# Performance work log

Measured on AMD Instinct MI355X. Metric: run time of the kernel, lower is better.

## Reference

```python
import jax, jax.numpy as jnp
import numpy as np

B, N, HID = 2, 2048, 1024
NH = 16
HD = HID // NH

def setup_inputs() -> dict:
    key = jax.random.key(0)
    ks = jax.random.split(key, 5)
    s = 0.02
    return {
        "hidden_states": jax.random.normal(ks[0], (B, N, HID), jnp.float32),
        "attention_mask": jnp.zeros((B, 1, 1, N), jnp.float32),
        "Wq": jax.random.normal(ks[1], (HID, HID), jnp.float32) * s,
        "bq": jnp.zeros((HID,), jnp.float32),
        "Wk": jax.random.normal(ks[2], (HID, HID), jnp.float32) * s,
        "bk": jnp.zeros((HID,), jnp.float32),
        "Wv": jax.random.normal(ks[3], (HID, HID), jnp.float32) * s,
        "bv": jnp.zeros((HID,), jnp.float32),
    }

def reference(hidden_states, attention_mask, Wq, bq, Wk, bk, Wv, bv):
    b, n, _ = hidden_states.shape
    def split_heads(t):  # [b,n,hid] -> [b,h,n,d]
        return t.reshape(b, n, NH, HD).transpose(0, 2, 1, 3)
    q = split_heads(hidden_states @ Wq.T + bq)
    k = split_heads(hidden_states @ Wk.T + bk)
    v = split_heads(hidden_states @ Wv.T + bv)
    scores = jnp.einsum('bhnd,bhmd->bhnm', q, k) / jnp.sqrt(jnp.float32(HD)).astype(q.dtype)
    scores = scores + attention_mask
    scores = jnp.maximum(scores, jnp.finfo(scores.dtype).min)
    probs = jax.nn.softmax(scores, axis=-1)
    out = jnp.einsum('bhnm,bhmd->bhnd', probs, v)
    return out.transpose(0, 2, 1, 3).reshape(b, n, NH * HD)
```

## Files before the change

### kernel.cpp

```cpp
#include <hip/hip_runtime.h>

typedef unsigned short u16;
typedef unsigned int   u32;
typedef __attribute__((ext_vector_type(8))) short bf16x8;
typedef __attribute__((ext_vector_type(4))) float f32x4;
typedef __attribute__((ext_vector_type(2))) unsigned int u32x2;

__device__ __forceinline__ float bf2f(u16 u) { return __uint_as_float(((u32)u) << 16); }
__device__ __forceinline__ u16 f2bf(float f) {
    return (u16)((__float_as_uint(f) + 0x8000u) >> 16);
}
__device__ __forceinline__ u32 cvt_pk_bf16(float lo, float hi) {
    u32 r;
    asm("v_cvt_pk_bf16_f32 %0, %1, %2" : "=v"(r) : "v"(lo), "v"(hi));
    return r;
}
__device__ __forceinline__ void gload16(const void* g, void* l) {
    __builtin_amdgcn_global_load_lds((const __attribute__((address_space(1))) void*)g,
                                     (__attribute__((address_space(3))) void*)l, 16, 0, 0);
}
#define VMCNT(n) asm volatile("s_waitcnt vmcnt(" #n ")" ::: "memory")

struct us4 { u16 x, y, z, w; };
__global__ void cvt_all(const float* __restrict__ hs, const float* __restrict__ wq,
                        const float* __restrict__ wk, const float* __restrict__ wv,
                        u16* __restrict__ dst)
{
    int i = blockIdx.x * blockDim.x + threadIdx.x;
    const int stride = gridDim.x * blockDim.x;
    us4* d4 = (us4*)dst;
    for (; i < 1835008; i += stride) {
        const float4* s4;
        int j = i;
        if (j < 1048576)      { s4 = (const float4*)hs; }
        else if (j < 1310720) { s4 = (const float4*)wq; j -= 1048576; }
        else if (j < 1572864) { s4 = (const float4*)wk; j -= 1310720; }
        else                  { s4 = (const float4*)wv; j -= 1572864; }
        float4 v = s4[j];
        us4 o;
        o.x = f2bf(v.x); o.y = f2bf(v.y); o.z = f2bf(v.z); o.w = f2bf(v.w);
        d4[i] = o;
    }
}

__global__ __launch_bounds__(256) void qkv_gemm(
    const u16* __restrict__ hs,
    const u16* __restrict__ Wq, const u16* __restrict__ Wk, const u16* __restrict__ Wv,
    const float* __restrict__ bq, const float* __restrict__ bk, const float* __restrict__ bv,
    u16* __restrict__ oq, u16* __restrict__ ok, u16* __restrict__ ovt)
{
    __shared__ u16 smem[32768];
    u16* sA0 = smem;
    u16* sB0 = smem + 8192;
    u16* sA1 = smem + 16384;
    u16* sB1 = smem + 24576;

    const int tid  = threadIdx.x;
    const int lane = tid & 63;
    const int w    = tid >> 6;
    const int c15  = lane & 15;
    const int q4   = lane >> 4;
    const int mat  = blockIdx.x >> 3;
    const int cb   = blockIdx.x & 7;
    const int rb   = blockIdx.y;
    const int wr   = w >> 1, wc = w & 1;

    const u16*   W    = (mat == 0) ? Wq : (mat == 1 ? Wk : Wv);
    const float* bias = (mat == 0) ? bq : (mat == 1 ? bk : bv);

    f32x4 acc[4][4] = {};

    const int rs = tid >> 3;
    const int cs = ((tid & 7) ^ (rs & 7)) * 8;
    const u16* gA = hs + (rb * 128) * 1024;
    const u16* gB = W + (cb * 128) * 1024;

    auto stageQ = [&](u16* dA, u16* dB, int kb) {
#pragma unroll
        for (int p = 0; p < 4; ++p)
            gload16(gA + (rs + 32 * p) * 1024 + kb + cs, dA + p * 2048 + w * 512);
#pragma unroll
        for (int p = 0; p < 4; ++p)
            gload16(gB + (rs + 32 * p) * 1024 + kb + cs, dB + p * 2048 + w * 512);
    };

    auto computeQ = [&](const u16* sA, const u16* sB) {
        __builtin_amdgcn_s_setprio(1);
#pragma unroll
        for (int kk = 0; kk < 2; ++kk) {
            const int cpos = ((kk * 4 + q4) ^ (c15 & 7)) * 8;
            bf16x8 af[4], bf[4];
#pragma unroll
            for (int mt = 0; mt < 4; ++mt)
                af[mt] = *(const bf16x8*)(sA + (wr * 64 + mt * 16 + c15) * 64 + cpos);
#pragma unroll
            for (int nt = 0; nt < 4; ++nt)
                bf[nt] = *(const bf16x8*)(sB + (wc * 64 + nt * 16 + c15) * 64 + cpos);
#pragma unroll
            for (int mt = 0; mt < 4; ++mt)
#pragma unroll
                for (int nt = 0; nt < 4; ++nt)
                    acc[mt][nt] = __builtin_amdgcn_mfma_f32_16x16x32_bf16(
                        af[mt], bf[nt], acc[mt][nt], 0, 0, 0);
        }
        __builtin_amdgcn_s_setprio(0);
    };

    stageQ(sA0, sB0, 0);
    stageQ(sA1, sB1, 64);

#pragma unroll 1
    for (int T = 0; T < 14; T += 2) {
        VMCNT(8);
        __builtin_amdgcn_s_barrier();
        __builtin_amdgcn_sched_barrier(0);
        computeQ(sA0, sB0);
        __builtin_amdgcn_s_barrier();
        __builtin_amdgcn_sched_barrier(0);
        stageQ(sA0, sB0, (T + 2) * 64);

        VMCNT(8);
        __builtin_amdgcn_s_barrier();
        __builtin_amdgcn_sched_barrier(0);
        computeQ(sA1, sB1);
        __builtin_amdgcn_s_barrier();
        __builtin_amdgcn_sched_barrier(0);
        stageQ(sA1, sB1, (T + 3) * 64);
    }
    VMCNT(8);
    __builtin_amdgcn_s_barrier();
    __builtin_amdgcn_sched_barrier(0);
    computeQ(sA0, sB0);
    VMCNT(0);
    __builtin_amdgcn_s_barrier();
    __builtin_amdgcn_sched_barrier(0);
    computeQ(sA1, sB1);

    __syncthreads();
    const int h = cb * 2 + wc;
    float bvv[4];
#pragma unroll
    for (int nt = 0; nt < 4; ++nt)
        bvv[nt] = bias[cb * 128 + wc * 64 + nt * 16 + c15];

    u16* sc = smem + w * 4608;
    if (mat != 2) {
        u16* dst = (mat == 0) ? oq : ok;
#pragma unroll
        for (int mt = 0; mt < 4; ++mt)
#pragma unroll
            for (int nt = 0; nt < 4; ++nt)
#pragma unroll
                for (int rr = 0; rr < 4; ++rr)
                    sc[(mt * 16 + q4 * 4 + rr) * 72 + nt * 16 + c15] =
                        f2bf(acc[mt][nt][rr] + bvv[nt]);
#pragma unroll
        for (int p = 0; p < 8; ++p) {
            const int s = p * 64 + lane;
            const int rl = s >> 3, oct = (s & 7) * 8;
            bf16x8 vv = *(const bf16x8*)(sc + rl * 72 + oct);
            const int n = rb * 128 + wr * 64 + rl;
            const int bb = n >> 11, nn = n & 2047;
            *(bf16x8*)(dst + (((bb * 16 + h) * 2048) + nn) * 64 + oct) = vv;
        }
    } else {
#pragma unroll
        for (int mt = 0; mt < 4; ++mt)
#pragma unroll
            for (int nt = 0; nt < 4; ++nt)
#pragma unroll
                for (int rr = 0; rr < 4; ++rr)
                    sc[(nt * 16 + c15) * 72 + mt * 16 + q4 * 4 + rr] =
                        f2bf(acc[mt][nt][rr] + bvv[nt]);
#pragma unroll
        for (int p = 0; p < 8; ++p) {
            const int s = p * 64 + lane;
            const int dr = s >> 3, noct = (s & 7) * 8;
            bf16x8 vv = *(const bf16x8*)(sc + dr * 72 + noct);
            const int n0 = rb * 128 + wr * 64 + noct;
            const int bb = n0 >> 11, nn = n0 & 2047;
            *(bf16x8*)(ovt + ((bb * 16 + h) * 64 + dr) * 2048 + nn) = vv;
        }
    }
}

__global__ __launch_bounds__(256, 2) void attn(
    const u16* __restrict__ qm, const u16* __restrict__ km, const u16* __restrict__ vtm,
    const float* __restrict__ mask, float* __restrict__ out)
{
    __shared__ u16 sK0[8192];
    __shared__ u16 sV0[8192];
    __shared__ u16 sK1[8192];
    __shared__ u16 sV1[8192];

    const int tid = threadIdx.x, lane = tid & 63, w = tid >> 6;
    const int c15 = lane & 15, q4 = lane >> 4;
    const int bh = blockIdx.x;
    const int qt = blockIdx.y;
    const int b = bh >> 4;

    bf16x8 qf[2][2];
    const u16* qbase = qm + (bh * 2048 + qt * 128 + w * 32) * 64;
#pragma unroll
    for (int rt = 0; rt < 2; ++rt)
#pragma unroll
        for (int kt = 0; kt < 2; ++kt)
            qf[rt][kt] = *(const bf16x8*)(qbase + (rt * 16 + c15) * 64 + kt * 32 + q4 * 8);

    float l_acc[2] = {0.f, 0.f};
    f32x4 accO[2][4] = {};

    const u16* kbase  = km  + bh * 2048 * 64;
    const u16* vtbase = vtm + bh * 64 * 2048;

    const int rK   = tid >> 3;
    const int colK = ((tid & 7) ^ (rK & 7)) * 8;
    const int prK  = (rK & 3) | ((rK & 0x0C) << 1) | ((rK & 0x10) >> 2);
    const int rV   = tid >> 4;
    const int colV = ((tid & 15) ^ (rV & 7)) * 8;
    const int ldsW = w * 512;

    const float* mbase = mask + b * 2048 + 8 * q4;

    auto stage = [&](u16* dK, u16* dV, int TT) {
        const u16* kg = kbase + TT * 128 * 64;
        const u16* vg = vtbase + TT * 128;
#pragma unroll
        for (int p = 0; p < 4; ++p)
            gload16(kg + (prK + 32 * p) * 64 + colK, dK + p * 2048 + ldsW);
#pragma unroll
        for (int p = 0; p < 4; ++p)
            gload16(vg + (rV + 16 * p) * 2048 + colV, dV + p * 2048 + ldsW);
    };

    auto compute64 = [&](const u16* sKh, const u16* sVb, int pcBase, int kb) {
        float mkv[4][4];
#pragma unroll
        for (int t = 0; t < 4; ++t) {
            float4 m4 = *(const float4*)(mbase + kb + 32 * (t >> 1) + 4 * (t & 1));
            mkv[t][0] = m4.x * 1.4426950408889634f;
            mkv[t][1] = m4.y * 1.4426950408889634f;
            mkv[t][2] = m4.z * 1.4426950408889634f;
            mkv[t][3] = m4.w * 1.4426950408889634f;
        }

        f32x4 accST[4][2] = {};
        __builtin_amdgcn_s_setprio(1);
#pragma unroll
        for (int kt = 0; kt < 2; ++kt) {
            bf16x8 kf[4];
#pragma unroll
            for (int t = 0; t < 4; ++t) {
                const int cpos = (kt * 4 + q4) ^ (c15 & 7);
                kf[t] = *(const bf16x8*)(sKh + (t * 16 + c15) * 64 + cpos * 8);
            }
#pragma unroll
            for (int t = 0; t < 4; ++t)
#pragma unroll
                for (int rt = 0; rt < 2; ++rt)
                    accST[t][rt] = __builtin_amdgcn_mfma_f32_16x16x32_bf16(
                        kf[t], qf[rt][kt], accST[t][rt], 0, 0, 0);
        }
        __builtin_amdgcn_s_setprio(0);

        u32 pu[4][2][2];
#pragma unroll
        for (int t = 0; t < 4; ++t)
#pragma unroll
            for (int rt = 0; rt < 2; ++rt) {
                float p[4];
#pragma unroll
                for (int rr = 0; rr < 4; ++rr) {
                    p[rr] = __builtin_amdgcn_exp2f(
                        fmaf(accST[t][rt][rr], 0.18033688011112042f, mkv[t][rr]));
                    l_acc[rt] += p[rr];
                }
                pu[t][rt][0] = cvt_pk_bf16(p[0], p[1]);
                pu[t][rt][1] = cvt_pk_bf16(p[2], p[3]);
            }

        __builtin_amdgcn_s_setprio(1);
#pragma unroll
        for (int g = 0; g < 2; ++g) {
            bf16x8 vB[4];
#pragma unroll
            for (int nt = 0; nt < 4; ++nt) {
                const int d = nt * 16 + c15;
                const int pc = pcBase + ((4 * g + q4) ^ (d & 7));
                vB[nt] = *(const bf16x8*)(sVb + d * 128 + pc * 8);
            }
#pragma unroll
            for (int rt = 0; rt < 2; ++rt) {
                union { bf16x8 v; u32 u[4]; } ta;
                ta.u[0] = pu[2 * g][rt][0];
                ta.u[1] = pu[2 * g][rt][1];
                ta.u[2] = pu[2 * g + 1][rt][0];
                ta.u[3] = pu[2 * g + 1][rt][1];
#pragma unroll
                for (int nt = 0; nt < 4; ++nt)
                    accO[rt][nt] = __builtin_amdgcn_mfma_f32_16x16x32_bf16(
                        ta.v, vB[nt], accO[rt][nt], 0, 0, 0);
            }
        }
        __builtin_amdgcn_s_setprio(0);
    };

    stage(sK0, sV0, 0);
    stage(sK1, sV1, 1);

#pragma unroll 1
    for (int T = 0; T < 14; T += 2) {
        VMCNT(8);
        __builtin_amdgcn_s_barrier();
        __builtin_amdgcn_sched_barrier(0);
        compute64(sK0, sV0, 0, T * 128);
        compute64(sK0 + 64 * 64, sV0, 8, T * 128 + 64);
        __builtin_amdgcn_s_barrier();
        __builtin_amdgcn_sched_barrier(0);
        stage(sK0, sV0, T + 2);

        VMCNT(8);
        __builtin_amdgcn_s_barrier();
        __builtin_amdgcn_sched_barrier(0);
        compute64(sK1, sV1, 0, (T + 1) * 128);
        compute64(sK1 + 64 * 64, sV1, 8, (T + 1) * 128 + 64);
        __builtin_amdgcn_s_barrier();
        __builtin_amdgcn_sched_barrier(0);
        stage(sK1, sV1, T + 3);
    }
    VMCNT(8);
    __builtin_amdgcn_s_barrier();
    __builtin_amdgcn_sched_barrier(0);
    compute64(sK0, sV0, 0, 14 * 128);
    compute64(sK0 + 64 * 64, sV0, 8, 14 * 128 + 64);
    VMCNT(0);
    __builtin_amdgcn_s_barrier();
    __builtin_amdgcn_sched_barrier(0);
    compute64(sK1, sV1, 0, 15 * 128);
    compute64(sK1 + 64 * 64, sV1, 8, 15 * 128 + 64);

#pragma unroll
    for (int rt = 0; rt < 2; ++rt) {
        l_acc[rt] += __shfl_xor(l_acc[rt], 16);
        l_acc[rt] += __shfl_xor(l_acc[rt], 32);
    }

    const int h = bh & 15;
#pragma unroll
    for (int rt = 0; rt < 2; ++rt) {
        float inv[4];
#pragma unroll
        for (int rr = 0; rr < 4; ++rr)
            inv[rr] = 1.0f / __shfl(l_acc[rt], q4 * 4 + rr);
#pragma unroll
        for (int nt = 0; nt < 4; ++nt)
#pragma unroll
            for (int rr = 0; rr < 4; ++rr) {
                const int qrow = qt * 128 + w * 32 + rt * 16 + q4 * 4 + rr;
                const int d = nt * 16 + c15;
                out[(b * 2048 + qrow) * 1024 + h * 64 + d] = accO[rt][nt][rr] * inv[rr];
            }
    }
}

extern "C" void kernel_launch(void* const* d_in, const int* in_sizes, int n_in,
                              void* d_out, int out_size, void* d_ws, size_t ws_size,
                              hipStream_t stream)
{
    const float* hs   = (const float*)d_in[0];
    const float* mask = (const float*)d_in[1];
    const float* Wq   = (const float*)d_in[2];
    const float* bq   = (const float*)d_in[3];
    const float* Wk   = (const float*)d_in[4];
    const float* bk   = (const float*)d_in[5];
    const float* Wv   = (const float*)d_in[6];
    const float* bv   = (const float*)d_in[7];

    u16* ws   = (u16*)d_ws;
    u16* qw   = ws;
    u16* kw   = ws + 4194304;
    u16* vtw  = ws + 8388608;
    u16* hsb  = ws + 12582912;
    u16* wqb  = ws + 16777216;
    u16* wkb  = ws + 17825792;
    u16* wvb  = ws + 18874368;

    cvt_all<<<1024, 256, 0, stream>>>(hs, Wq, Wk, Wv, hsb);

    qkv_gemm<<<dim3(24, 32), 256, 0, stream>>>(hsb, wqb, wkb, wvb, bq, bk, bv, qw, kw, vtw);
    attn<<<dim3(32, 16), 256, 0, stream>>>(qw, kw, vtw, mask, (float*)d_out);
}
```

Baseline: 162.3 us.

## Shrink attention blocks to 128 threads with 64-query, 64-key tiles

The attention kernel now uses two waves per block covering 64 query rows instead of four waves covering 128. The launch grid doubles to 1024 blocks. K/V tiles shrink to 64 keys per stage, which halves LDS per block and doubles the number of pipeline iterations. The aim is more blocks in flight and better CU occupancy and load balance. In exchange, each block runs twice as many barriers and staging rounds, and K/V get reloaded from global/L2 twice as often in total. The exp sum is also reassociated into a pairwise add.

```diff
diff --git a/kernel.cpp b/kernel.cpp
--- a/kernel.cpp
+++ b/kernel.cpp
@@ -4,7 +4,6 @@
 typedef unsigned int   u32;
 typedef __attribute__((ext_vector_type(8))) short bf16x8;
 typedef __attribute__((ext_vector_type(4))) float f32x4;
-typedef __attribute__((ext_vector_type(2))) unsigned int u32x2;
 
 __device__ __forceinline__ float bf2f(u16 u) { return __uint_as_float(((u32)u) << 16); }
 __device__ __forceinline__ u16 f2bf(float f) {
@@ -184,14 +183,14 @@
     }
 }
 
-__global__ __launch_bounds__(256, 2) void attn(
+__global__ __launch_bounds__(128, 2) void attn(
     const u16* __restrict__ qm, const u16* __restrict__ km, const u16* __restrict__ vtm,
     const float* __restrict__ mask, float* __restrict__ out)
 {
-    __shared__ u16 sK0[8192];
-    __shared__ u16 sV0[8192];
-    __shared__ u16 sK1[8192];
-    __shared__ u16 sV1[8192];
+    __shared__ u16 sK0[4096];
+    __shared__ u16 sV0[4096];
+    __shared__ u16 sK1[4096];
+    __shared__ u16 sV1[4096];
 
     const int tid = threadIdx.x, lane = tid & 63, w = tid >> 6;
     const int c15 = lane & 15, q4 = lane >> 4;
@@ -200,7 +199,7 @@
     const int b = bh >> 4;
 
     bf16x8 qf[2][2];
-    const u16* qbase = qm + (bh * 2048 + qt * 128 + w * 32) * 64;
+    const u16* qbase = qm + (bh * 2048 + qt * 64 + w * 32) * 64;
 #pragma unroll
     for (int rt = 0; rt < 2; ++rt)
 #pragma unroll
@@ -213,27 +212,31 @@
     const u16* kbase  = km  + bh * 2048 * 64;
     const u16* vtbase = vtm + bh * 64 * 2048;
 
-    const int rK   = tid >> 3;
-    const int colK = ((tid & 7) ^ (rK & 7)) * 8;
-    const int prK  = (rK & 3) | ((rK & 0x0C) << 1) | ((rK & 0x10) >> 2);
-    const int rV   = tid >> 4;
-    const int colV = ((tid & 15) ^ (rV & 7)) * 8;
-    const int ldsW = w * 512;
+    const int rs  = tid >> 3;
+    const int col = ((tid & 7) ^ (rs & 7)) * 8;
+    int prK[4], rV[4];
+#pragma unroll
+    for (int p = 0; p < 4; ++p) {
+        const int row = 16 * p + rs;
+        prK[p] = (row & 0x23) | ((row & 0x0C) << 1) | ((row & 0x10) >> 2);
+        rV[p]  = row;
+    }
+    const int ldsO = w * 512;
 
     const float* mbase = mask + b * 2048 + 8 * q4;
 
     auto stage = [&](u16* dK, u16* dV, int TT) {
-        const u16* kg = kbase + TT * 128 * 64;
-        const u16* vg = vtbase + TT * 128;
+        const u16* kg = kbase + TT * 64 * 64;
+        const u16* vg = vtbase + TT * 64;
 #pragma unroll
         for (int p = 0; p < 4; ++p)
-            gload16(kg + (prK + 32 * p) * 64 + colK, dK + p * 2048 + ldsW);
+            gload16(kg + prK[p] * 64 + col, dK + p * 1024 + ldsO);
 #pragma unroll
         for (int p = 0; p < 4; ++p)
-            gload16(vg + (rV + 16 * p) * 2048 + colV, dV + p * 2048 + ldsW);
+            gload16(vg + rV[p] * 2048 + col, dV + p * 1024 + ldsO);
     };
 
-    auto compute64 = [&](const u16* sKh, const u16* sVb, int pcBase, int kb) {
+    auto compute64 = [&](const u16* sKh, const u16* sVT, int kb) {
         float mkv[4][4];
 #pragma unroll
         for (int t = 0; t < 4; ++t) {
@@ -251,8 +254,9 @@
             bf16x8 kf[4];
 #pragma unroll
             for (int t = 0; t < 4; ++t) {
-                const int cpos = (kt * 4 + q4) ^ (c15 & 7);
-                kf[t] = *(const bf16x8*)(sKh + (t * 16 + c15) * 64 + cpos * 8);
+                const int rho = t * 16 + c15;
+                const int cpos = (kt * 4 + q4) ^ (rho & 7);
+                kf[t] = *(const bf16x8*)(sKh + rho * 64 + cpos * 8);
             }
 #pragma unroll
             for (int t = 0; t < 4; ++t)
@@ -268,15 +272,17 @@
         for (int t = 0; t < 4; ++t)
 #pragma unroll
             for (int rt = 0; rt < 2; ++rt) {
-                float p[4];
-#pragma unroll
-                for (int rr = 0; rr < 4; ++rr) {
-                    p[rr] = __builtin_amdgcn_exp2f(
-                        fmaf(accST[t][rt][rr], 0.18033688011112042f, mkv[t][rr]));
-                    l_acc[rt] += p[rr];
-                }
-                pu[t][rt][0] = cvt_pk_bf16(p[0], p[1]);
-                pu[t][rt][1] = cvt_pk_bf16(p[2], p[3]);
+                float p0 = __builtin_amdgcn_exp2f(
+                    fmaf(accST[t][rt][0], 0.18033688011112042f, mkv[t][0]));
+                float p1 = __builtin_amdgcn_exp2f(
+                    fmaf(accST[t][rt][1], 0.18033688011112042f, mkv[t][1]));
+                float p2 = __builtin_amdgcn_exp2f(
+                    fmaf(accST[t][rt][2], 0.18033688011112042f, mkv[t][2]));
+                float p3 = __builtin_amdgcn_exp2f(
+                    fmaf(accST[t][rt][3], 0.18033688011112042f, mkv[t][3]));
+                l_acc[rt] += (p0 + p1) + (p2 + p3);
+                pu[t][rt][0] = cvt_pk_bf16(p0, p1);
+                pu[t][rt][1] = cvt_pk_bf16(p2, p3);
             }
 
         __builtin_amdgcn_s_setprio(1);
@@ -286,8 +292,8 @@
 #pragma unroll
             for (int nt = 0; nt < 4; ++nt) {
                 const int d = nt * 16 + c15;
-                const int pc = pcBase + ((4 * g + q4) ^ (d & 7));
-                vB[nt] = *(const bf16x8*)(sVb + d * 128 + pc * 8);
+                const int pc = (4 * g + q4) ^ (d & 7);
+                vB[nt] = *(const bf16x8*)(sVT + d * 64 + pc * 8);
             }
 #pragma unroll
             for (int rt = 0; rt < 2; ++rt) {
@@ -309,12 +315,11 @@
     stage(sK1, sV1, 1);
 
 #pragma unroll 1
-    for (int T = 0; T < 14; T += 2) {
+    for (int T = 0; T < 30; T += 2) {
         VMCNT(8);
         __builtin_amdgcn_s_barrier();
         __builtin_amdgcn_sched_barrier(0);
-        compute64(sK0, sV0, 0, T * 128);
-        compute64(sK0 + 64 * 64, sV0, 8, T * 128 + 64);
+        compute64(sK0, sV0, T * 64);
         __builtin_amdgcn_s_barrier();
         __builtin_amdgcn_sched_barrier(0);
         stage(sK0, sV0, T + 2);
@@ -322,8 +327,7 @@
         VMCNT(8);
         __builtin_amdgcn_s_barrier();
         __builtin_amdgcn_sched_barrier(0);
-        compute64(sK1, sV1, 0, (T + 1) * 128);
-        compute64(sK1 + 64 * 64, sV1, 8, (T + 1) * 128 + 64);
+        compute64(sK1, sV1, (T + 1) * 64);
         __builtin_amdgcn_s_barrier();
         __builtin_amdgcn_sched_barrier(0);
         stage(sK1, sV1, T + 3);
@@ -331,13 +335,11 @@
     VMCNT(8);
     __builtin_amdgcn_s_barrier();
     __builtin_amdgcn_sched_barrier(0);
-    compute64(sK0, sV0, 0, 14 * 128);
-    compute64(sK0 + 64 * 64, sV0, 8, 14 * 128 + 64);
+    compute64(sK0, sV0, 30 * 64);
     VMCNT(0);
     __builtin_amdgcn_s_barrier();
     __builtin_amdgcn_sched_barrier(0);
-    compute64(sK1, sV1, 0, 15 * 128);
-    compute64(sK1 + 64 * 64, sV1, 8, 15 * 128 + 64);
+    compute64(sK1, sV1, 31 * 64);
 
 #pragma unroll
     for (int rt = 0; rt < 2; ++rt) {
@@ -356,7 +358,7 @@
         for (int nt = 0; nt < 4; ++nt)
 #pragma unroll
             for (int rr = 0; rr < 4; ++rr) {
-                const int qrow = qt * 128 + w * 32 + rt * 16 + q4 * 4 + rr;
+                const int qrow = qt * 64 + w * 32 + rt * 16 + q4 * 4 + rr;
                 const int d = nt * 16 + c15;
                 out[(b * 2048 + qrow) * 1024 + h * 64 + d] = accO[rt][nt][rr] * inv[rr];
             }
@@ -388,5 +390,5 @@
     cvt_all<<<1024, 256, 0, stream>>>(hs, Wq, Wk, Wv, hsb);
 
     qkv_gemm<<<dim3(24, 32), 256, 0, stream>>>(hsb, wqb, wkb, wvb, bq, bk, bv, qw, kw, vtw);
-    attn<<<dim3(32, 16), 256, 0, stream>>>(qw, kw, vtw, mask, (float*)d_out);
-}
+    attn<<<dim3(32, 32), 128, 0, stream>>>(qw, kw, vtw, mask, (float*)d_out);
+}
```

Result: slower. 173.8 us (+7.1%).
